# Performance work log

Measured on AMD Instinct MI355X. Metric: run time of the kernel, lower is better.

The kernel has to match this reference:

```python
import jax, jax.numpy as jnp
import numpy as np

H = 1024
HEADS = 16
FFN = 2048
EPS = 1e-5


def _layernorm(x, g, b):
    mu = jnp.mean(x, axis=-1, keepdims=True)
    var = jnp.mean(jnp.square(x - mu), axis=-1, keepdims=True)
    return (x - mu) * jax.lax.rsqrt(var + EPS) * g + b


def setup_inputs() -> dict:
    key = jax.random.key(0)
    ks = jax.random.split(key, 8)
    N, L = 4, 1024
    s = 1.0 / np.sqrt(H)
    inp = {
        "src_hidden": jax.random.normal(ks[0], (N, L, H), dtype=jnp.float32),
        "src_mask": jnp.ones((N, L), dtype=jnp.int32),
        "Wq": jax.random.normal(ks[1], (H, H), dtype=jnp.float32) * s,
        "bq": jnp.zeros((H,), jnp.float32),
        "Wk": jax.random.normal(ks[2], (H, H), dtype=jnp.float32) * s,
        "bk": jnp.zeros((H,), jnp.float32),
        "Wv": jax.random.normal(ks[3], (H, H), dtype=jnp.float32) * s,
        "bv": jnp.zeros((H,), jnp.float32),
        "Wo": jax.random.normal(ks[4], (H, H), dtype=jnp.float32) * s,
        "bo": jnp.zeros((H,), jnp.float32),
        "ln1_g": jnp.ones((H,), jnp.float32),
        "ln1_b": jnp.zeros((H,), jnp.float32),
        "W1": jax.random.normal(ks[5], (H, FFN), dtype=jnp.float32) * s,
        "b1": jnp.zeros((FFN,), jnp.float32),
        "W2": jax.random.normal(ks[6], (FFN, H), dtype=jnp.float32) * (1.0 / np.sqrt(FFN)),
        "b2": jnp.zeros((H,), jnp.float32),
        "ln2_g": jnp.ones((H,), jnp.float32),
        "ln2_b": jnp.zeros((H,), jnp.float32),
    }
    return inp


def reference(src_hidden, src_mask, Wq, bq, Wk, bk, Wv, bv, Wo, bo,
              ln1_g, ln1_b, W1, b1, W2, b2, ln2_g, ln2_b):
    N, L, _ = src_hidden.shape
    d = H // HEADS
    scale = 1.0 / np.sqrt(H)  # applied to BOTH Q and K, as in the original
    # NOTE: head split is a plain reshape (view), faithful to the original code
    Q = ((src_hidden @ Wq + bq).reshape(N, HEADS, L, d)) * scale
    K = ((src_hidden @ Wk + bk).reshape(N, HEADS, L, d)) * scale
    V = (src_hidden @ Wv + bv).reshape(N, HEADS, L, d)
    sims = jnp.einsum('nhid,nhjd->nhij', Q, K)  # (N, heads, L, L)
    mask = src_mask[:, None, None, :]  # (N,1,1,L) broadcasts over heads and query dim
    sims = jnp.where(mask == 0, -jnp.inf, sims)
    attn = jax.nn.softmax(sims, axis=-1)
    ctx = jnp.einsum('nhij,nhjd->nhid', attn, V)
    concats = ctx.reshape(N, L, H)
    hid = concats @ Wo + bo
    x1 = _layernorm(hid, ln1_g, ln1_b) + hid
    ffn = jax.nn.relu(x1 @ W1 + b1) @ W2 + b2  # dropout is identity in eval
    out = _layernorm(ffn, ln2_g, ln2_b) + ffn
    return (out, src_mask)
```

## Files before the change

### kernel.cpp

```cpp
#include <hip/hip_runtime.h>
#include <math.h>

#define H 1024
#define HEADS 16
#define DH 64
#define FFN_DIM 2048
#define EPS 1e-5f
#define NB 4
#define LL 1024
#define M_ROWS 4096

typedef __attribute__((ext_vector_type(8))) short bf16x8;
typedef __attribute__((ext_vector_type(4))) float f32x4;

__device__ __forceinline__ ushort f2bf(float x) {
    union { float f; unsigned u; } c; c.f = x;
    unsigned u = c.u;
    u += 0x7FFFu + ((u >> 16) & 1u);
    return (ushort)(u >> 16);
}

__device__ __forceinline__ unsigned pack2bf(float a, float b) {
    union { float f; unsigned u; } ca, cb; ca.f = a; cb.f = b;
    const unsigned ua = ca.u + 0x8000u;
    const unsigned ub = cb.u + 0x8000u;
    return (ua >> 16) | (ub & 0xFFFF0000u);
}

#define GLL(gp, lp)                                                         \
    __builtin_amdgcn_global_load_lds(                                       \
        (const __attribute__((address_space(1))) void*)(gp),                \
        (__attribute__((address_space(3))) void*)(lp), 16, 0, 0)

#define WAITV4() asm volatile("s_waitcnt vmcnt(4)" ::: "memory")
#define WAITV0() asm volatile("s_waitcnt vmcnt(0)" ::: "memory")
#define BAR() __builtin_amdgcn_s_barrier()

__global__ __launch_bounds__(512, 4)
void gemm_bf16(const ushort* __restrict__ A, const ushort* __restrict__ Bt,
               const float* __restrict__ bias, float* __restrict__ Cf,
               ushort* __restrict__ Cb, int M, int N, int K,
               int relu, int qkv)
{
    __shared__ ushort As[2][128 * 64];
    __shared__ ushort Bs[2][128 * 64];
    const int tid = threadIdx.x;
    const int l = tid & 63, w = tid >> 6;
    const int h  = w >> 2;
    const int wr = (w >> 1) & 1, wc = w & 1;
    const int g = l >> 4, c0 = l & 15;
    const int brow = blockIdx.y * 128, bcol = blockIdx.x * 128;
    const int NS = K >> 6;

    const ushort* Abase = A + (size_t)brow * K;
    const ushort* Bbase = Bt + (size_t)bcol * K;

    f32x4 acc[4][4];
    #pragma unroll
    for (int mi = 0; mi < 4; ++mi)
        #pragma unroll
        for (int ni = 0; ni < 4; ++ni)
            acc[mi][ni] = (f32x4)0.0f;

    auto stage = [&](int buf, int k0) {
        #pragma unroll
        for (int i = 0; i < 2; ++i) {
            const int f = i * 512 + tid;
            const int row = f >> 3, p = f & 7;
            const int c = p ^ (row & 7);
            const ushort* ga = Abase + (size_t)row * K + k0 + c * 8;
            const ushort* gb = Bbase + (size_t)row * K + k0 + c * 8;
            ushort* la = As[buf] + (size_t)(i * 512 + w * 64) * 8;
            ushort* lb = Bs[buf] + (size_t)(i * 512 + w * 64) * 8;
            GLL(ga, la);
            GLL(gb, lb);
        }
    };

    stage(0, 0);
    int cur = 0;
    for (int t = 0; t < NS; ++t) {
        if (t + 1 < NS) { stage(cur ^ 1, (t + 1) << 6); WAITV4(); }
        else            { WAITV0(); }
        BAR();

        bf16x8 af[4], bf[4];
        #pragma unroll
        for (int mi = 0; mi < 4; ++mi) {
            const int row = wr * 64 + mi * 16 + c0;
            const int cc = (h * 4 + g) ^ (row & 7);
            af[mi] = *(const bf16x8*)&As[cur][row * 64 + cc * 8];
        }
        #pragma unroll
        for (int ni = 0; ni < 4; ++ni) {
            const int row = wc * 64 + ni * 16 + c0;
            const int cc = (h * 4 + g) ^ (row & 7);
            bf[ni] = *(const bf16x8*)&Bs[cur][row * 64 + cc * 8];
        }
        __builtin_amdgcn_s_setprio(1);
        #pragma unroll
        for (int mi = 0; mi < 4; ++mi)
            #pragma unroll
            for (int ni = 0; ni < 4; ++ni)
                acc[mi][ni] = __builtin_amdgcn_mfma_f32_16x16x32_bf16(
                    af[mi], bf[ni], acc[mi][ni], 0, 0, 0);
        __builtin_amdgcn_s_setprio(0);
        BAR();
        cur ^= 1;
    }

    if (h == 1) {
        const int u = w - 4;
        f32x4* zone = (u & 2) ? (f32x4*)Bs : (f32x4*)As;
        const int uu = u & 1;
        #pragma unroll
        for (int mi = 0; mi < 4; ++mi)
            #pragma unroll
            for (int ni = 0; ni < 4; ++ni)
                zone[(size_t)((uu * 16 + mi * 4 + ni) * 64 + l)] = acc[mi][ni];
    }
    __syncthreads();
    if (h == 1) return;

    {
        f32x4* zone = (w & 2) ? (f32x4*)Bs : (f32x4*)As;
        const int uu = w & 1;
        #pragma unroll
        for (int mi = 0; mi < 4; ++mi)
            #pragma unroll
            for (int ni = 0; ni < 4; ++ni) {
                f32x4 p = zone[(size_t)((uu * 16 + mi * 4 + ni) * 64 + l)];
                acc[mi][ni] += p;
            }
    }

    const int colg0 = bcol + wc * 64 + c0;
    const int rbase = brow + wr * 64 + (g << 2);
    const int seg   = qkv ? (bcol >> 10) : 0;
    const int Nw    = qkv ? 1024 : N;
    ushort* outb    = qkv ? (Cb + (size_t)seg * 4194304u) : Cb;
    #pragma unroll
    for (int ni = 0; ni < 4; ++ni) {
        const int colg = colg0 + ni * 16;
        const int colw = qkv ? (colg & 1023) : colg;
        const float bv = bias[colg];
        #pragma unroll
        for (int mi = 0; mi < 4; ++mi) {
            #pragma unroll
            for (int j = 0; j < 4; ++j) {
                float v = acc[mi][ni][j] + bv;
                if (relu) v = fmaxf(v, 0.0f);
                const size_t off = (size_t)(rbase + mi * 16 + j) * Nw + colw;
                if (Cf) Cf[off] = v;
                if (Cb) outb[off] = f2bf(v);
            }
        }
    }
}

__global__ __launch_bounds__(256)
void prep(const float* __restrict__ X, ushort* __restrict__ Xb,
          const float* __restrict__ Wq, const float* __restrict__ Wk,
          const float* __restrict__ Wv, const float* __restrict__ Wo,
          const float* __restrict__ W1, const float* __restrict__ W2,
          ushort* __restrict__ Wqkvt, ushort* __restrict__ Wot,
          ushort* __restrict__ W1t, ushort* __restrict__ W2t,
          const float* __restrict__ bq, const float* __restrict__ bk,
          const float* __restrict__ bv, float* __restrict__ biasqkv,
          const int* __restrict__ mask, int* __restrict__ mfl,
          float* __restrict__ maskout)
{
    const int b = blockIdx.x;
    const int tid = threadIdx.x;

    if (b < 4096) {
        const int i = b * 256 + tid;
        float4 v = *reinterpret_cast<const float4*>(&X[(size_t)i * 4]);
        ushort4 o;
        o.x = f2bf(v.x); o.y = f2bf(v.y); o.z = f2bf(v.z); o.w = f2bf(v.w);
        *reinterpret_cast<ushort4*>(&Xb[(size_t)i * 4]) = o;
        return;
    }
    int r = b - 4096;
    const float* W = nullptr; ushort* D = nullptr;
    int K = H, N = H; float sc = 1.0f; int blin = 0;
    if (r < 4096) {
        const int which = r >> 10;
        blin = r & 1023;
        switch (which) {
            case 0: W = Wq; D = Wqkvt;               sc = 0.03125f; break;
            case 1: W = Wk; D = Wqkvt + 1024 * 1024; sc = 0.03125f; break;
            case 2: W = Wv; D = Wqkvt + 2048 * 1024; sc = 1.0f;     break;
            default: W = Wo; D = Wot;                sc = 1.0f;     break;
        }
    } else if (r < 4096 + 2048) {
        W = W1; D = W1t; K = H; N = FFN_DIM; blin = r - 4096;
    } else if (r < 4096 + 4096) {
        W = W2; D = W2t; K = FFN_DIM; N = H; blin = r - 4096 - 2048;
    }
    if (W) {
        __shared__ float t[32][33];
        const int nbx = N >> 5;
        const int bx = blin % nbx, by = blin / nbx;
        const int n0 = bx * 32, k0 = by * 32;
        const int tx = tid & 31, ty = tid >> 5;
        #pragma unroll
        for (int rr = 0; rr < 4; ++rr)
            t[ty + rr * 8][tx] = W[(size_t)(k0 + ty + rr * 8) * N + n0 + tx];
        __syncthreads();
        #pragma unroll
        for (int rr = 0; rr < 4; ++rr)
            D[(size_t)(n0 + ty + rr * 8) * K + k0 + tx] =
                f2bf(t[tx][ty + rr * 8] * sc);
        return;
    }
    r -= 8192;
    if (r < 12) {
        const int i = r * 256 + tid;
        if (i < 3072) {
            float v;
            if (i < 1024) v = bq[i] * 0.03125f;
            else if (i < 2048) v = bk[i - 1024] * 0.03125f;
            else v = bv[i - 2048];
            biasqkv[i] = v;
        }
        return;
    }
    if (r == 12) {
        if (tid < NB * 16) {
            const int n = tid >> 4, tile = tid & 15;
            int any = 0;
            for (int j = 0; j < 64; ++j)
                any |= (mask[n * LL + tile * 64 + j] == 0);
            mfl[tid] = any;
        }
        return;
    }
    {
        const int i = (r - 13) * 256 + tid;
        if (i < NB * LL) maskout[i] = (float)mask[i];
    }
}

__global__ __launch_bounds__(256)
void transpose_v(const ushort* __restrict__ V, ushort* __restrict__ Vt)
{
    const int nh = blockIdx.y, jt = blockIdx.x;
    const size_t base = (size_t)nh << 16;
    __shared__ ushort t[64][68];
    const int tid = threadIdx.x;
    #pragma unroll
    for (int pass = 0; pass < 4; ++pass) {
        const int j = pass * 16 + (tid >> 4);
        const int d0 = (tid & 15) * 4;
        ushort4 v = *(const ushort4*)&V[base + (size_t)(jt * 64 + j) * 64 + d0];
        t[d0 + 0][j] = v.x; t[d0 + 1][j] = v.y;
        t[d0 + 2][j] = v.z; t[d0 + 3][j] = v.w;
    }
    __syncthreads();
    #pragma unroll
    for (int pass = 0; pass < 4; ++pass) {
        const int d = pass * 16 + (tid >> 4);
        const int j0 = (tid & 15) * 4;
        ushort4 o;
        o.x = t[d][j0 + 0]; o.y = t[d][j0 + 1];
        o.z = t[d][j0 + 2]; o.w = t[d][j0 + 3];
        *(ushort4*)&Vt[base + (size_t)d * 1024 + jt * 64 + j0] = o;
    }
}

__global__ __launch_bounds__(256)
void attn_mfma(const ushort* __restrict__ Q, const ushort* __restrict__ K,
               const ushort* __restrict__ Vt, const int* __restrict__ mask,
               const int* __restrict__ mflags, ushort* __restrict__ ctx)
{
    const int nh = blockIdx.y;
    const int n  = nh >> 4;
    const int qb = blockIdx.x;
    const size_t hb = (size_t)nh << 16;
    const ushort* Qh = Q + hb;
    const ushort* Kh = K + hb;
    const ushort* Vh = Vt + hb;
    ushort* Ch = ctx + hb;

    __shared__ ushort Ks[2][64 * 64];
    __shared__ ushort Vs[2][64 * 64];
    __shared__ ushort Ps[4][16 * 64];

    const int tid = threadIdx.x;
    const int l = tid & 63, w = tid >> 6;
    const int g = l >> 4, c0 = l & 15;
    const int fsw = (c0 & 7) << 1;

    unsigned fbits = 0;
    #pragma unroll
    for (int tt = 0; tt < 16; ++tt)
        fbits |= (unsigned)(mflags[n * 16 + tt] != 0) << tt;

    const ushort* qrow = Qh + (size_t)(qb * 64 + w * 16 + c0) * 64;
    const bf16x8 qf0 = *(const bf16x8*)(qrow + g * 8);
    const bf16x8 qf1 = *(const bf16x8*)(qrow + 32 + g * 8);

    f32x4 Oacc[4];
    #pragma unroll
    for (int nd = 0; nd < 4; ++nd) Oacc[nd] = (f32x4)0.0f;
    float lp = 0.0f;

    auto stage = [&](int buf, int t) {
        #pragma unroll
        for (int i = 0; i < 2; ++i) {
            const int slot = i * 256 + tid;
            const int r = slot >> 3, p = slot & 7;
            const int c = p ^ (r & 7);
            const ushort* gk = Kh + (size_t)(t * 64 + r) * 64 + c * 8;
            const ushort* gv = Vh + (size_t)r * 1024 + t * 64 + c * 8;
            ushort* lk = Ks[buf] + (size_t)(i * 256 + w * 64) * 8;
            ushort* lv = Vs[buf] + (size_t)(i * 256 + w * 64) * 8;
            GLL(gk, lk);
            GLL(gv, lv);
        }
    };

    stage(0, 0);
    int cur = 0;
    for (int t = 0; t < 16; ++t) {
        if (t < 15) { stage(cur ^ 1, t + 1); WAITV4(); }
        else        { WAITV0(); }
        BAR();

        f32x4 s[4];
        #pragma unroll
        for (int nb = 0; nb < 4; ++nb) {
            s[nb] = (f32x4)0.0f;
            const int row = nb * 16 + c0;
            const int cc0 = g ^ (row & 7);
            const int cc1 = (4 + g) ^ (row & 7);
            bf16x8 kf0 = *(const bf16x8*)&Ks[cur][row * 64 + cc0 * 8];
            bf16x8 kf1 = *(const bf16x8*)&Ks[cur][row * 64 + cc1 * 8];
            __builtin_amdgcn_s_setprio(1);
            s[nb] = __builtin_amdgcn_mfma_f32_16x16x32_bf16(kf0, qf0, s[nb], 0, 0, 0);
            s[nb] = __builtin_amdgcn_mfma_f32_16x16x32_bf16(kf1, qf1, s[nb], 0, 0, 0);
            __builtin_amdgcn_s_setprio(0);
        }
        if (fbits >> t & 1) {
            #pragma unroll
            for (int nb = 0; nb < 4; ++nb)
                #pragma unroll
                for (int jr = 0; jr < 4; ++jr) {
                    const int key = 16 * nb + 4 * g + jr;
                    if (mask[n * LL + t * 64 + key] == 0)
                        s[nb][jr] = -INFINITY;
                }
        }
        #pragma unroll
        for (int nb = 0; nb < 4; ++nb)
            #pragma unroll
            for (int jr = 0; jr < 4; ++jr) {
                const float pv = __expf(s[nb][jr]);
                s[nb][jr] = pv;
                lp += pv;
            }

        ushort* Pw = Ps[w];
        #pragma unroll
        for (int nb = 0; nb < 4; ++nb) {
            const int gi = (4 * nb + g) ^ fsw;
            uint2 pk;
            pk.x = pack2bf(s[nb][0], s[nb][1]);
            pk.y = pack2bf(s[nb][2], s[nb][3]);
            *(uint2*)&Pw[c0 * 64 + gi * 4] = pk;
        }
        const bf16x8 pa0 = *(const bf16x8*)&Pw[c0 * 64 + ((2 * g) ^ fsw) * 4];
        const bf16x8 pa1 = *(const bf16x8*)&Pw[c0 * 64 + ((8 + 2 * g) ^ fsw) * 4];
        #pragma unroll
        for (int nd = 0; nd < 4; ++nd) {
            const int row = nd * 16 + c0;
            const int cc0 = g ^ (row & 7);
            const int cc1 = (4 + g) ^ (row & 7);
            bf16x8 vf0 = *(const bf16x8*)&Vs[cur][row * 64 + cc0 * 8];
            bf16x8 vf1 = *(const bf16x8*)&Vs[cur][row * 64 + cc1 * 8];
            __builtin_amdgcn_s_setprio(1);
            Oacc[nd] = __builtin_amdgcn_mfma_f32_16x16x32_bf16(pa0, vf0, Oacc[nd], 0, 0, 0);
            Oacc[nd] = __builtin_amdgcn_mfma_f32_16x16x32_bf16(pa1, vf1, Oacc[nd], 0, 0, 0);
            __builtin_amdgcn_s_setprio(0);
        }
        BAR();
        cur ^= 1;
    }

    float v = lp;
    v += __shfl_xor(v, 16, 64);
    v += __shfl_xor(v, 32, 64);
    float invq[4];
    #pragma unroll
    for (int jr = 0; jr < 4; ++jr) {
        const int src = 20 * g + jr;
        invq[jr] = 1.0f / __shfl(v, src, 64);
    }
    #pragma unroll
    for (int nd = 0; nd < 4; ++nd) {
        #pragma unroll
        for (int jr = 0; jr < 4; ++jr) {
            const int row = qb * 64 + w * 16 + 4 * g + jr;
            Ch[(size_t)row * 64 + nd * 16 + c0] = f2bf(Oacc[nd][jr] * invq[jr]);
        }
    }
}

__global__ __launch_bounds__(256)
void ln_residual(const float* __restrict__ X, const float* __restrict__ X2,
                 const float* __restrict__ g, const float* __restrict__ b,
                 float* __restrict__ outf, ushort* __restrict__ outb)
{
    const int row = blockIdx.x;
    const int tid = threadIdx.x;
    float4 xv = *reinterpret_cast<const float4*>(&X[(size_t)row * H + tid * 4]);
    if (X2) {
        float4 yv = *reinterpret_cast<const float4*>(&X2[(size_t)row * H + tid * 4]);
        xv.x += yv.x; xv.y += yv.y; xv.z += yv.z; xv.w += yv.w;
    }
    float s = xv.x + xv.y + xv.z + xv.w;
    __shared__ float red[8];
    const int lane = tid & 63, wave = tid >> 6;
    #pragma unroll
    for (int off = 32; off > 0; off >>= 1) s += __shfl_down(s, off);
    if (lane == 0) red[wave] = s;
    __syncthreads();
    if (tid == 0)
        red[0] = (red[0] + red[1] + red[2] + red[3]) * (1.0f / H);
    __syncthreads();
    const float mu = red[0];
    const float d0 = xv.x - mu, d1 = xv.y - mu, d2 = xv.z - mu, d3 = xv.w - mu;
    float s2 = d0 * d0 + d1 * d1 + d2 * d2 + d3 * d3;
    #pragma unroll
    for (int off = 32; off > 0; off >>= 1) s2 += __shfl_down(s2, off);
    if (lane == 0) red[4 + wave] = s2;
    __syncthreads();
    if (tid == 0) {
        const float var = (red[4] + red[5] + red[6] + red[7]) * (1.0f / H);
        red[4] = rsqrtf(var + EPS);
    }
    __syncthreads();
    const float rstd = red[4];
    float4 gv = *reinterpret_cast<const float4*>(&g[tid * 4]);
    float4 bv = *reinterpret_cast<const float4*>(&b[tid * 4]);
    float4 ov;
    ov.x = d0 * rstd * gv.x + bv.x + xv.x;
    ov.y = d1 * rstd * gv.y + bv.y + xv.y;
    ov.z = d2 * rstd * gv.z + bv.z + xv.z;
    ov.w = d3 * rstd * gv.w + bv.w + xv.w;
    if (outf)
        *reinterpret_cast<float4*>(&outf[(size_t)row * H + tid * 4]) = ov;
    if (outb) {
        ushort4 ob;
        ob.x = f2bf(ov.x); ob.y = f2bf(ov.y);
        ob.z = f2bf(ov.z); ob.w = f2bf(ov.w);
        *reinterpret_cast<ushort4*>(&outb[(size_t)row * H + tid * 4]) = ob;
    }
}

extern "C" void kernel_launch(void* const* d_in, const int* in_sizes, int n_in,
                              void* d_out, int out_size, void* d_ws, size_t ws_size,
                              hipStream_t stream)
{
    const float* X    = (const float*)d_in[0];
    const int*   mask = (const int*)d_in[1];
    const float* Wq   = (const float*)d_in[2];
    const float* bq   = (const float*)d_in[3];
    const float* Wk   = (const float*)d_in[4];
    const float* bk   = (const float*)d_in[5];
    const float* Wv   = (const float*)d_in[6];
    const float* bv   = (const float*)d_in[7];
    const float* Wo   = (const float*)d_in[8];
    const float* bo   = (const float*)d_in[9];
    const float* g1   = (const float*)d_in[10];
    const float* bln1 = (const float*)d_in[11];
    const float* W1   = (const float*)d_in[12];
    const float* b1   = (const float*)d_in[13];
    const float* W2   = (const float*)d_in[14];
    const float* b2   = (const float*)d_in[15];
    const float* g2   = (const float*)d_in[16];
    const float* bln2 = (const float*)d_in[17];

    char* wsb = (char*)d_ws;
    const size_t MB = 1u << 20;
    ushort* Qb16 = (ushort*)(wsb);
    ushort* Vb16 = (ushort*)(wsb + 16 * MB);
    ushort* Xb   = (ushort*)(wsb + 24 * MB);
    ushort* ctxb = (ushort*)(wsb + 24 * MB);
    ushort* Vtb  = (ushort*)(wsb + 32 * MB);
    ushort* x1b  = (ushort*)(wsb + 32 * MB);
    ushort* Wqkvt = (ushort*)(wsb + 40 * MB);
    ushort* Wot   = (ushort*)(wsb + 46 * MB);
    ushort* W1t   = (ushort*)(wsb + 48 * MB);
    ushort* W2t   = (ushort*)(wsb + 52 * MB);
    float*  biasqkv = (float*)(wsb + 56 * MB);
    int*    mfl     = (int*)(wsb + 56 * MB + 16384);
    float*  hid = (float*)(wsb);
    ushort* Fb  = (ushort*)(wsb + 16 * MB);
    float*  ffn = (float*)(wsb);

    dim3 blk(256), gblk(512);

    prep<<<dim3(4096 + 4096 + 2048 + 2048 + 12 + 1 + 16), blk, 0, stream>>>(
        X, Xb, Wq, Wk, Wv, Wo, W1, W2, Wqkvt, Wot, W1t, W2t,
        bq, bk, bv, biasqkv, mask, mfl,
        (float*)d_out + (size_t)M_ROWS * H);

    gemm_bf16<<<dim3(24, 32), gblk, 0, stream>>>(
        Xb, Wqkvt, biasqkv, nullptr, Qb16, M_ROWS, 3072, H, 0, 1);
    transpose_v<<<dim3(16, NB * HEADS), blk, 0, stream>>>(Vb16, Vtb);

    attn_mfma<<<dim3(16, NB * HEADS), blk, 0, stream>>>(
        Qb16, Qb16 + 4194304u, Vtb, mask, mfl, ctxb);

    gemm_bf16<<<dim3(8, 32), gblk, 0, stream>>>(
        ctxb, Wot, bo, hid, nullptr, M_ROWS, H, H, 0, 0);
    ln_residual<<<dim3(M_ROWS), blk, 0, stream>>>(hid, nullptr, g1, bln1,
                                                  nullptr, x1b);

    gemm_bf16<<<dim3(16, 32), gblk, 0, stream>>>(
        x1b, W1t, b1, nullptr, Fb, M_ROWS, FFN_DIM, H, 1, 0);
    gemm_bf16<<<dim3(8, 32), gblk, 0, stream>>>(
        Fb, W2t, b2, ffn, nullptr, M_ROWS, H, FFN_DIM, 0, 0);

    ln_residual<<<dim3(M_ROWS), blk, 0, stream>>>(ffn, nullptr, g2, bln2,
                                                  (float*)d_out, nullptr);
}
```

Baseline: 199.8 us.

## Split-K GEMMs with triple-buffered K=32 stages and direct-global attention loads

Reworks the GEMM to use 8 warps each owning a 64x32 output tile with K-step 32 and a three-stage LDS ring, replacing the intra-block K-split reduction. Adds a grid-level split-K (z=2) for the Wo and W2 GEMMs, writing two float partials that ln_residual sums, to raise block count on the narrow-N GEMMs. The attention kernel drops LDS staging of K/V and reads fragments straight from global memory, removing barriers but relying on cache hits. Workspace layout is reshuffled to fit the partial buffers.

```diff
diff --git a/kernel.cpp b/kernel.cpp
--- a/kernel.cpp
+++ b/kernel.cpp
@@ -33,117 +33,95 @@
         (__attribute__((address_space(3))) void*)(lp), 16, 0, 0)
 
 #define WAITV4() asm volatile("s_waitcnt vmcnt(4)" ::: "memory")
+#define WAITV2() asm volatile("s_waitcnt vmcnt(2)" ::: "memory")
 #define WAITV0() asm volatile("s_waitcnt vmcnt(0)" ::: "memory")
 #define BAR() __builtin_amdgcn_s_barrier()
 
-__global__ __launch_bounds__(512, 4)
+__global__ __launch_bounds__(512, 6)
 void gemm_bf16(const ushort* __restrict__ A, const ushort* __restrict__ Bt,
-               const float* __restrict__ bias, float* __restrict__ Cf,
-               ushort* __restrict__ Cb, int M, int N, int K,
-               int relu, int qkv)
-{
-    __shared__ ushort As[2][128 * 64];
-    __shared__ ushort Bs[2][128 * 64];
+               const float* __restrict__ bias, float* __restrict__ Cf0,
+               float* __restrict__ Cf1, ushort* __restrict__ Cb,
+               int M, int N, int K, int relu, int qkv)
+{
+    __shared__ ushort As[3][128 * 32];
+    __shared__ ushort Bs[3][128 * 32];
     const int tid = threadIdx.x;
     const int l = tid & 63, w = tid >> 6;
-    const int h  = w >> 2;
-    const int wr = (w >> 1) & 1, wc = w & 1;
+    const int wr = w >> 2, wc = w & 3;
     const int g = l >> 4, c0 = l & 15;
     const int brow = blockIdx.y * 128, bcol = blockIdx.x * 128;
-    const int NS = K >> 6;
-
-    const ushort* Abase = A + (size_t)brow * K;
-    const ushort* Bbase = Bt + (size_t)bcol * K;
-
-    f32x4 acc[4][4];
+    const int z = blockIdx.z;
+    const int Ksub = K / gridDim.z;
+    const int NS = Ksub >> 5;
+
+    const ushort* Abase = A + (size_t)brow * K + (size_t)z * Ksub;
+    const ushort* Bbase = Bt + (size_t)bcol * K + (size_t)z * Ksub;
+
+    f32x4 acc[4][2];
     #pragma unroll
     for (int mi = 0; mi < 4; ++mi)
         #pragma unroll
-        for (int ni = 0; ni < 4; ++ni)
+        for (int ni = 0; ni < 2; ++ni)
             acc[mi][ni] = (f32x4)0.0f;
 
     auto stage = [&](int buf, int k0) {
-        #pragma unroll
-        for (int i = 0; i < 2; ++i) {
-            const int f = i * 512 + tid;
-            const int row = f >> 3, p = f & 7;
-            const int c = p ^ (row & 7);
-            const ushort* ga = Abase + (size_t)row * K + k0 + c * 8;
-            const ushort* gb = Bbase + (size_t)row * K + k0 + c * 8;
-            ushort* la = As[buf] + (size_t)(i * 512 + w * 64) * 8;
-            ushort* lb = Bs[buf] + (size_t)(i * 512 + w * 64) * 8;
-            GLL(ga, la);
-            GLL(gb, lb);
-        }
+        const int row = tid >> 2, cp = tid & 3;
+        const int c = cp ^ ((row >> 1) & 3);
+        const ushort* ga = Abase + (size_t)row * K + k0 + c * 8;
+        const ushort* gb = Bbase + (size_t)row * K + k0 + c * 8;
+        ushort* la = As[buf] + (size_t)w * 512;
+        ushort* lb = Bs[buf] + (size_t)w * 512;
+        GLL(ga, la);
+        GLL(gb, lb);
     };
 
     stage(0, 0);
-    int cur = 0;
+    stage(1, 32);
+    int scur = 0;
     for (int t = 0; t < NS; ++t) {
-        if (t + 1 < NS) { stage(cur ^ 1, (t + 1) << 6); WAITV4(); }
-        else            { WAITV0(); }
+        int snext = scur + 2; if (snext >= 3) snext -= 3;
+        if (t + 2 < NS) stage(snext, (t + 2) << 5);
+        if (t < NS - 2)       WAITV4();
+        else if (t == NS - 2) WAITV2();
+        else                  WAITV0();
         BAR();
 
-        bf16x8 af[4], bf[4];
+        bf16x8 af[4], bf[2];
         #pragma unroll
         for (int mi = 0; mi < 4; ++mi) {
             const int row = wr * 64 + mi * 16 + c0;
-            const int cc = (h * 4 + g) ^ (row & 7);
-            af[mi] = *(const bf16x8*)&As[cur][row * 64 + cc * 8];
-        }
-        #pragma unroll
-        for (int ni = 0; ni < 4; ++ni) {
-            const int row = wc * 64 + ni * 16 + c0;
-            const int cc = (h * 4 + g) ^ (row & 7);
-            bf[ni] = *(const bf16x8*)&Bs[cur][row * 64 + cc * 8];
+            const int cc = g ^ ((row >> 1) & 3);
+            af[mi] = *(const bf16x8*)&As[scur][row * 32 + cc * 8];
+        }
+        #pragma unroll
+        for (int ni = 0; ni < 2; ++ni) {
+            const int row = wc * 32 + ni * 16 + c0;
+            const int cc = g ^ ((row >> 1) & 3);
+            bf[ni] = *(const bf16x8*)&Bs[scur][row * 32 + cc * 8];
         }
         __builtin_amdgcn_s_setprio(1);
         #pragma unroll
         for (int mi = 0; mi < 4; ++mi)
             #pragma unroll
-            for (int ni = 0; ni < 4; ++ni)
+            for (int ni = 0; ni < 2; ++ni)
                 acc[mi][ni] = __builtin_amdgcn_mfma_f32_16x16x32_bf16(
                     af[mi], bf[ni], acc[mi][ni], 0, 0, 0);
         __builtin_amdgcn_s_setprio(0);
         BAR();
-        cur ^= 1;
-    }
-
-    if (h == 1) {
-        const int u = w - 4;
-        f32x4* zone = (u & 2) ? (f32x4*)Bs : (f32x4*)As;
-        const int uu = u & 1;
-        #pragma unroll
-        for (int mi = 0; mi < 4; ++mi)
-            #pragma unroll
-            for (int ni = 0; ni < 4; ++ni)
-                zone[(size_t)((uu * 16 + mi * 4 + ni) * 64 + l)] = acc[mi][ni];
-    }
-    __syncthreads();
-    if (h == 1) return;
-
-    {
-        f32x4* zone = (w & 2) ? (f32x4*)Bs : (f32x4*)As;
-        const int uu = w & 1;
-        #pragma unroll
-        for (int mi = 0; mi < 4; ++mi)
-            #pragma unroll
-            for (int ni = 0; ni < 4; ++ni) {
-                f32x4 p = zone[(size_t)((uu * 16 + mi * 4 + ni) * 64 + l)];
-                acc[mi][ni] += p;
-            }
-    }
-
-    const int colg0 = bcol + wc * 64 + c0;
+        scur = scur + 1 == 3 ? 0 : scur + 1;
+    }
+
+    float* Cf = (z == 0) ? Cf0 : Cf1;
+    const int colg0 = bcol + wc * 32 + c0;
     const int rbase = brow + wr * 64 + (g << 2);
     const int seg   = qkv ? (bcol >> 10) : 0;
     const int Nw    = qkv ? 1024 : N;
     ushort* outb    = qkv ? (Cb + (size_t)seg * 4194304u) : Cb;
     #pragma unroll
-    for (int ni = 0; ni < 4; ++ni) {
+    for (int ni = 0; ni < 2; ++ni) {
         const int colg = colg0 + ni * 16;
         const int colw = qkv ? (colg & 1023) : colg;
-        const float bv = bias[colg];
+        const float bv = (z == 0) ? bias[colg] : 0.0f;
         #pragma unroll
         for (int mi = 0; mi < 4; ++mi) {
             #pragma unroll
@@ -283,8 +261,6 @@
     const ushort* Vh = Vt + hb;
     ushort* Ch = ctx + hb;
 
-    __shared__ ushort Ks[2][64 * 64];
-    __shared__ ushort Vs[2][64 * 64];
     __shared__ ushort Ps[4][16 * 64];
 
     const int tid = threadIdx.x;
@@ -306,37 +282,14 @@
     for (int nd = 0; nd < 4; ++nd) Oacc[nd] = (f32x4)0.0f;
     float lp = 0.0f;
 
-    auto stage = [&](int buf, int t) {
-        #pragma unroll
-        for (int i = 0; i < 2; ++i) {
-            const int slot = i * 256 + tid;
-            const int r = slot >> 3, p = slot & 7;
-            const int c = p ^ (r & 7);
-            const ushort* gk = Kh + (size_t)(t * 64 + r) * 64 + c * 8;
-            const ushort* gv = Vh + (size_t)r * 1024 + t * 64 + c * 8;
-            ushort* lk = Ks[buf] + (size_t)(i * 256 + w * 64) * 8;
-            ushort* lv = Vs[buf] + (size_t)(i * 256 + w * 64) * 8;
-            GLL(gk, lk);
-            GLL(gv, lv);
-        }
-    };
-
-    stage(0, 0);
-    int cur = 0;
     for (int t = 0; t < 16; ++t) {
-        if (t < 15) { stage(cur ^ 1, t + 1); WAITV4(); }
-        else        { WAITV0(); }
-        BAR();
-
         f32x4 s[4];
         #pragma unroll
         for (int nb = 0; nb < 4; ++nb) {
             s[nb] = (f32x4)0.0f;
-            const int row = nb * 16 + c0;
-            const int cc0 = g ^ (row & 7);
-            const int cc1 = (4 + g) ^ (row & 7);
-            bf16x8 kf0 = *(const bf16x8*)&Ks[cur][row * 64 + cc0 * 8];
-            bf16x8 kf1 = *(const bf16x8*)&Ks[cur][row * 64 + cc1 * 8];
+            const ushort* krow = Kh + (size_t)(t * 64 + nb * 16 + c0) * 64;
+            bf16x8 kf0 = *(const bf16x8*)(krow + g * 8);
+            bf16x8 kf1 = *(const bf16x8*)(krow + 32 + g * 8);
             __builtin_amdgcn_s_setprio(1);
             s[nb] = __builtin_amdgcn_mfma_f32_16x16x32_bf16(kf0, qf0, s[nb], 0, 0, 0);
             s[nb] = __builtin_amdgcn_mfma_f32_16x16x32_bf16(kf1, qf1, s[nb], 0, 0, 0);
@@ -374,18 +327,14 @@
         const bf16x8 pa1 = *(const bf16x8*)&Pw[c0 * 64 + ((8 + 2 * g) ^ fsw) * 4];
         #pragma unroll
         for (int nd = 0; nd < 4; ++nd) {
-            const int row = nd * 16 + c0;
-            const int cc0 = g ^ (row & 7);
-            const int cc1 = (4 + g) ^ (row & 7);
-            bf16x8 vf0 = *(const bf16x8*)&Vs[cur][row * 64 + cc0 * 8];
-            bf16x8 vf1 = *(const bf16x8*)&Vs[cur][row * 64 + cc1 * 8];
+            const ushort* vrow = Vh + (size_t)(nd * 16 + c0) * 1024 + t * 64;
+            bf16x8 vf0 = *(const bf16x8*)(vrow + g * 8);
+            bf16x8 vf1 = *(const bf16x8*)(vrow + 32 + g * 8);
             __builtin_amdgcn_s_setprio(1);
             Oacc[nd] = __builtin_amdgcn_mfma_f32_16x16x32_bf16(pa0, vf0, Oacc[nd], 0, 0, 0);
             Oacc[nd] = __builtin_amdgcn_mfma_f32_16x16x32_bf16(pa1, vf1, Oacc[nd], 0, 0, 0);
             __builtin_amdgcn_s_setprio(0);
         }
-        BAR();
-        cur ^= 1;
     }
 
     float v = lp;
@@ -484,21 +433,22 @@
 
     char* wsb = (char*)d_ws;
     const size_t MB = 1u << 20;
-    ushort* Qb16 = (ushort*)(wsb);
-    ushort* Vb16 = (ushort*)(wsb + 16 * MB);
-    ushort* Xb   = (ushort*)(wsb + 24 * MB);
-    ushort* ctxb = (ushort*)(wsb + 24 * MB);
-    ushort* Vtb  = (ushort*)(wsb + 32 * MB);
-    ushort* x1b  = (ushort*)(wsb + 32 * MB);
-    ushort* Wqkvt = (ushort*)(wsb + 40 * MB);
-    ushort* Wot   = (ushort*)(wsb + 46 * MB);
-    ushort* W1t   = (ushort*)(wsb + 48 * MB);
-    ushort* W2t   = (ushort*)(wsb + 52 * MB);
-    float*  biasqkv = (float*)(wsb + 56 * MB);
-    int*    mfl     = (int*)(wsb + 56 * MB + 16384);
-    float*  hid = (float*)(wsb);
-    ushort* Fb  = (ushort*)(wsb + 16 * MB);
-    float*  ffn = (float*)(wsb);
+    ushort* Qb16  = (ushort*)(wsb);
+    ushort* ctxb  = (ushort*)(wsb + 16 * MB);
+    ushort* x1b   = (ushort*)(wsb + 16 * MB);
+    ushort* Xb    = (ushort*)(wsb + 24 * MB);
+    ushort* Vtb   = (ushort*)(wsb + 32 * MB);
+    ushort* W1t   = (ushort*)(wsb + 40 * MB);
+    ushort* Wot   = (ushort*)(wsb + 44 * MB);
+    float*  biasqkv = (float*)(wsb + 46 * MB);
+    int*    mfl     = (int*)(wsb + 46 * MB + 16384);
+    ushort* W2t   = (ushort*)(wsb + 48 * MB);
+    ushort* Wqkvt = (ushort*)(wsb + 52 * MB);
+    float*  P0 = (float*)(wsb);
+    float*  P1 = (float*)(wsb + 24 * MB);
+    ushort* Fb = (ushort*)(wsb);
+    float*  Q0 = (float*)(wsb + 16 * MB);
+    float*  Q1 = (float*)(wsb + 32 * MB);
 
     dim3 blk(256), gblk(512);
 
@@ -507,23 +457,24 @@
         bq, bk, bv, biasqkv, mask, mfl,
         (float*)d_out + (size_t)M_ROWS * H);
 
-    gemm_bf16<<<dim3(24, 32), gblk, 0, stream>>>(
-        Xb, Wqkvt, biasqkv, nullptr, Qb16, M_ROWS, 3072, H, 0, 1);
-    transpose_v<<<dim3(16, NB * HEADS), blk, 0, stream>>>(Vb16, Vtb);
+    gemm_bf16<<<dim3(24, 32, 1), gblk, 0, stream>>>(
+        Xb, Wqkvt, biasqkv, nullptr, nullptr, Qb16, M_ROWS, 3072, H, 0, 1);
+    transpose_v<<<dim3(16, NB * HEADS), blk, 0, stream>>>(
+        Qb16 + 2u * 4194304u, Vtb);
 
     attn_mfma<<<dim3(16, NB * HEADS), blk, 0, stream>>>(
         Qb16, Qb16 + 4194304u, Vtb, mask, mfl, ctxb);
 
-    gemm_bf16<<<dim3(8, 32), gblk, 0, stream>>>(
-        ctxb, Wot, bo, hid, nullptr, M_ROWS, H, H, 0, 0);
-    ln_residual<<<dim3(M_ROWS), blk, 0, stream>>>(hid, nullptr, g1, bln1,
+    gemm_bf16<<<dim3(8, 32, 2), gblk, 0, stream>>>(
+        ctxb, Wot, bo, P0, P1, nullptr, M_ROWS, H, H, 0, 0);
+    ln_residual<<<dim3(M_ROWS), blk, 0, stream>>>(P0, P1, g1, bln1,
                                                   nullptr, x1b);
 
-    gemm_bf16<<<dim3(16, 32), gblk, 0, stream>>>(
-        x1b, W1t, b1, nullptr, Fb, M_ROWS, FFN_DIM, H, 1, 0);
-    gemm_bf16<<<dim3(8, 32), gblk, 0, stream>>>(
-        Fb, W2t, b2, ffn, nullptr, M_ROWS, H, FFN_DIM, 0, 0);
-
-    ln_residual<<<dim3(M_ROWS), blk, 0, stream>>>(ffn, nullptr, g2, bln2,
+    gemm_bf16<<<dim3(16, 32, 1), gblk, 0, stream>>>(
+        x1b, W1t, b1, nullptr, nullptr, Fb, M_ROWS, FFN_DIM, H, 1, 0);
+    gemm_bf16<<<dim3(8, 32, 2), gblk, 0, stream>>>(
+        Fb, W2t, b2, Q0, Q1, nullptr, M_ROWS, H, FFN_DIM, 0, 0);
+
+    ln_residual<<<dim3(M_ROWS), blk, 0, stream>>>(Q0, Q1, g2, bln2,
                                                   (float*)d_out, nullptr);
 }
```

Measured after the change: 265.9 us. +33.1%, slower.
